# Optimization experiments

Measured on AMD Instinct MI355X. Metric: run time of the kernel, lower is better.

## Reference

```python
import jax, jax.numpy as jnp
import numpy as np

N, F, H, C = 8192, 512, 512, 64
SPARSITY = 0.5  # args.linear_sparsity


def _percentile(t, q):
    # torch kthvalue semantics: k = 1 + round(0.01*q*(n-1)), 1-indexed k-th smallest
    n = t.size
    k = int(1 + round(0.01 * q * (n - 1)))
    return jnp.sort(t.ravel())[k - 1]


def _pair_norm(x):
    x = x - x.mean(axis=0)
    rownorm_mean = jnp.sqrt(1e-6 + (x * x).sum(axis=1).mean())
    return x / rownorm_mean


def setup_inputs() -> dict:
    key = jax.random.key(0)
    ks = jax.random.split(key, 8)
    x = jax.random.normal(ks[0], (N, F), jnp.float32)
    adj = (jax.random.uniform(ks[1], (N, N)) < 0.002).astype(jnp.float32)
    W0 = jax.random.normal(ks[2], (H, F), jnp.float32) * (1.0 / np.sqrt(F))
    W1 = jax.random.normal(ks[3], (H, H), jnp.float32) * (1.0 / np.sqrt(H))
    W2 = jax.random.normal(ks[4], (C, H), jnp.float32) * (1.0 / np.sqrt(H))
    S0 = jax.random.normal(ks[5], (H, F), jnp.float32)
    S1 = jax.random.normal(ks[6], (H, H), jnp.float32)
    S2 = jax.random.normal(ks[7], (C, H), jnp.float32)
    return {"x": x, "adj": adj, "W0": W0, "W1": W1, "W2": W2,
            "S0": S0, "S1": S1, "S2": S2}


def reference(x, adj, W0, W1, W2, S0, S1, S2):
    # add self loops
    idx = jnp.arange(N)
    adj = adj.at[idx, idx].set(1.0)
    # global threshold over all |score| params (enable_abs_comp=True)
    all_scores = jnp.concatenate([jnp.abs(S0).ravel(), jnp.abs(S1).ravel(), jnp.abs(S2).ravel()])
    thr = _percentile(all_scores, SPARSITY * 100.0)
    # symmetric normalization D^-1/2 A D^-1/2
    deg_inv_sqrt = jnp.maximum(adj.sum(axis=-1), 1.0) ** -0.5
    adj_n = deg_inv_sqrt[:, None] * adj * deg_inv_sqrt[None, :]

    def masked_linear(h, W, S):
        Wm = W * (jnp.abs(S) > thr).astype(W.dtype)
        return h @ Wm.T

    # layers 0..num_layers-2 applied back-to-back (as in the source loop)
    h = masked_linear(x, W0, S0)
    h = masked_linear(h, W1, S1)
    h = adj_n @ h            # aggregation: [N,N] @ [N,H]
    h = _pair_norm(h)
    h = jax.nn.relu(h)
    h = masked_linear(h, W2, S2)
    return adj_n @ h          # [N, C]
```

## Files before the change

### kernel.cpp

```cpp
#include <hip/hip_runtime.h>
#include <hip/hip_bf16.h>

#define NN 8192
#define FF 512
#define HH 512
#define CC 64
#define NS_TOTAL 557056
#define KSEL 278529u
#define MAXNBR 96
#define MASKB 2176

typedef short short8 __attribute__((ext_vector_type(8)));
typedef __bf16 bf16x8 __attribute__((ext_vector_type(8)));
typedef float f32x4 __attribute__((ext_vector_type(4)));

__device__ inline unsigned short f2bf(float f) {
    unsigned u = __float_as_uint(f);
    u += 0x7fffu + ((u >> 16) & 1u);
    return (unsigned short)(u >> 16);
}
__device__ inline float bf2f(unsigned short h) {
    return __uint_as_float(((unsigned)h) << 16);
}

__device__ inline f32x4 mfma16x16x32(short8 a, short8 b, f32x4 c) {
    return __builtin_amdgcn_mfma_f32_16x16x32_bf16(
        __builtin_bit_cast(bf16x8, a), __builtin_bit_cast(bf16x8, b), c, 0, 0, 0);
}

__device__ inline void gload_lds16(const unsigned short* g, unsigned short* l) {
    __builtin_amdgcn_global_load_lds(
        (const __attribute__((address_space(1))) void*)g,
        (__attribute__((address_space(3))) void*)l,
        16, 0, 0);
}

__device__ void isel(const unsigned* __restrict__ hist, unsigned k,
                     unsigned& bin, unsigned& krem) {
    __shared__ unsigned sh[256];
    __shared__ unsigned res[2];
    const int t = threadIdx.x;
    __syncthreads();
    sh[t] = hist[t];
    __syncthreads();
    unsigned pre = 0;
    for (int i = 0; i < t; ++i) pre += sh[i];
    if (pre < k && k <= pre + sh[t]) { res[0] = (unsigned)t; res[1] = k - pre; }
    __syncthreads();
    bin = res[0]; krem = res[1];
}

__device__ void isel_chain(const unsigned* __restrict__ hists, int npass,
                           unsigned& prefix, unsigned& k) {
    prefix = 0; k = KSEL;
    for (int p = 0; p < npass; ++p) {
        unsigned bin, krem;
        isel(hists + p * 256, k, bin, krem);
        prefix |= bin << (24 - 8 * p);
        k = krem;
    }
}


__global__ __launch_bounds__(256) void hist8_kernel(const float* __restrict__ S0,
                                                    const float* __restrict__ S1,
                                                    const float* __restrict__ S2,
                                                    unsigned* __restrict__ hists, int pass) {
    unsigned prefix = 0, k;
    if (pass > 0) isel_chain(hists, pass, prefix, k);
    unsigned pmask = (pass > 0) ? (0xFFFFFFFFu << (32 - 8 * pass)) : 0u;
    int shift = 24 - 8 * pass;
    __shared__ unsigned lh[256];
    lh[threadIdx.x] = 0;
    __syncthreads();
    int stride = gridDim.x * blockDim.x;
    for (int idx = blockIdx.x * blockDim.x + threadIdx.x; idx < NS_TOTAL; idx += stride) {
        float v = (idx < 262144) ? S0[idx] : (idx < 524288) ? S1[idx - 262144] : S2[idx - 524288];
        unsigned key = __float_as_uint(fabsf(v));
        if ((key & pmask) == prefix)
            atomicAdd(&lh[(key >> shift) & 0xffu], 1u);
    }
    __syncthreads();
    unsigned c = lh[threadIdx.x];
    if (c) atomicAdd(&hists[pass * 256 + threadIdx.x], c);
}


__global__ __launch_bounds__(256) void mask_split_fused(
        const float* __restrict__ W0, const float* __restrict__ W1,
        const float* __restrict__ W2, const float* __restrict__ S0,
        const float* __restrict__ S1, const float* __restrict__ S2,
        const unsigned* __restrict__ hists,
        unsigned short* __restrict__ W0h, unsigned short* __restrict__ W0l,
        unsigned short* __restrict__ W1h, unsigned short* __restrict__ W1l,
        unsigned short* __restrict__ W2h, unsigned short* __restrict__ W2l,
        const float* __restrict__ X,
        unsigned short* __restrict__ Xh, unsigned short* __restrict__ Xl) {
    if (blockIdx.x >= MASKB) {
        int i = (blockIdx.x - MASKB) * 256 + threadIdx.x;
        float4 v = ((const float4*)X)[i];
        float vv[4] = {v.x, v.y, v.z, v.w};
        ushort4 hi, lo;
        unsigned short* hp = (unsigned short*)&hi;
        unsigned short* lp = (unsigned short*)&lo;
#pragma unroll
        for (int j = 0; j < 4; ++j) {
            hp[j] = f2bf(vv[j]);
            lp[j] = f2bf(vv[j] - bf2f(hp[j]));
        }
        *(ushort4*)&Xh[(size_t)i * 4] = hi;
        *(ushort4*)&Xl[(size_t)i * 4] = lo;
        return;
    }
    unsigned prefix, k;
    isel_chain(hists, 4, prefix, k);
    float thr = __uint_as_float(prefix);
    int idx = blockIdx.x * 256 + threadIdx.x;
    const float* W; const float* S; unsigned short* Yh; unsigned short* Yl; int i;
    if (idx < 262144)      { W = W0; S = S0; Yh = W0h; Yl = W0l; i = idx; }
    else if (idx < 524288) { W = W1; S = S1; Yh = W1h; Yl = W1l; i = idx - 262144; }
    else                   { W = W2; S = S2; Yh = W2h; Yl = W2l; i = idx - 524288; }
    float v = (fabsf(S[i]) > thr) ? W[i] : 0.f;
    unsigned short hi = f2bf(v);
    Yh[i] = hi;
    Yl[i] = f2bf(v - bf2f(hi));
}


template<int BMt, int BNt, int WRITE_SPLIT>
__global__ __launch_bounds__(256) void gemm_hl(
        const unsigned short* __restrict__ Ah, const unsigned short* __restrict__ Al,
        const unsigned short* __restrict__ Bh, const unsigned short* __restrict__ Bl,
        float* __restrict__ Cf, unsigned short* __restrict__ Ch,
        unsigned short* __restrict__ Cl, int Nn, int gridN, int gemmBlocks,
        const float* __restrict__ adj, int* __restrict__ nnz, int* __restrict__ colsI,
        float* __restrict__ dis, int degRow0) {
    constexpr int BK = 32;
    constexpr int MF = BMt / 32, NF = BNt / 32;
    __shared__ __align__(16) unsigned short AhS[BMt * BK], AlS[BMt * BK];
    __shared__ __align__(16) unsigned short BhS[BNt * BK], BlS[BNt * BK];
    __shared__ int dcnt;

    if ((int)blockIdx.x >= gemmBlocks) {
        int row = degRow0 + (int)blockIdx.x - gemmBlocks;
        if (threadIdx.x == 0) dcnt = 0;
        __syncthreads();
        const float4* arow = (const float4*)(adj + (size_t)row * NN);
        int* cp = colsI + (size_t)row * MAXNBR;
        for (int c4 = threadIdx.x; c4 < NN / 4; c4 += 256) {
            float4 v = arow[c4];
            int base = c4 * 4;
            float vv[4] = {v.x, v.y, v.z, v.w};
#pragma unroll
            for (int kq = 0; kq < 4; ++kq) {
                int col = base + kq;
                if (vv[kq] != 0.f || col == row) {
                    int s = atomicAdd(&dcnt, 1);
                    if (s < MAXNBR) cp[s] = col;
                }
            }
        }
        __syncthreads();
        if (threadIdx.x == 0) {
            int c = dcnt;
            nnz[row] = (c < MAXNBR) ? c : MAXNBR;
            dis[row] = rsqrtf((float)c);
        }
        return;
    }
    const int tid = threadIdx.x, lane = tid & 63, wid = tid >> 6;
    const int wr = wid >> 1, wc = wid & 1;
    const int bm = ((int)blockIdx.x / gridN) * BMt;
    const int bn = ((int)blockIdx.x % gridN) * BNt;
    const int r16 = lane & 15, kg = lane >> 4;
    const int srow = lane >> 2, scol = (lane & 3) * 8;
    constexpr int cA = BMt / 16, cB = BNt / 16, CPW = (2 * cA + 2 * cB) / 4;
    f32x4 acc[MF][NF] = {};

    for (int k0 = 0; k0 < 512; k0 += BK) {
        __syncthreads();
#pragma unroll
        for (int i = 0; i < CPW; ++i) {
            int c = wid * CPW + i;
            const unsigned short* src; unsigned short* dst; int cc, r0;
            if (c < cA)               { src = Ah; dst = AhS; cc = c;              r0 = bm + cc * 16; }
            else if (c < 2 * cA)      { src = Al; dst = AlS; cc = c - cA;         r0 = bm + cc * 16; }
            else if (c < 2 * cA + cB) { src = Bh; dst = BhS; cc = c - 2 * cA;     r0 = bn + cc * 16; }
            else                      { src = Bl; dst = BlS; cc = c - 2 * cA - cB; r0 = bn + cc * 16; }
            gload_lds16(src + (size_t)(r0 + srow) * 512 + k0 + scol, dst + cc * 512);
        }
        __syncthreads();
        const unsigned short* pAh = &AhS[(wr * (BMt / 2) + r16) * BK + kg * 8];
        const unsigned short* pAl = &AlS[(wr * (BMt / 2) + r16) * BK + kg * 8];
        const unsigned short* pBh = &BhS[(wc * (BNt / 2) + r16) * BK + kg * 8];
        const unsigned short* pBl = &BlS[(wc * (BNt / 2) + r16) * BK + kg * 8];
        short8 bh[NF], bl[NF];
#pragma unroll
        for (int n = 0; n < NF; ++n) {
            bh[n] = *(const short8*)(pBh + n * 16 * BK);
            bl[n] = *(const short8*)(pBl + n * 16 * BK);
        }
#pragma unroll
        for (int m = 0; m < MF; ++m) {
            short8 ah = *(const short8*)(pAh + m * 16 * BK);
            short8 al = *(const short8*)(pAl + m * 16 * BK);
#pragma unroll
            for (int n = 0; n < NF; ++n) {
                acc[m][n] = mfma16x16x32(ah, bh[n], acc[m][n]);
                acc[m][n] = mfma16x16x32(ah, bl[n], acc[m][n]);
                acc[m][n] = mfma16x16x32(al, bh[n], acc[m][n]);
            }
        }
    }
#pragma unroll
    for (int m = 0; m < MF; ++m) {
#pragma unroll
        for (int n = 0; n < NF; ++n) {
            int row0 = bm + wr * (BMt / 2) + m * 16 + kg * 4;
            int col  = bn + wc * (BNt / 2) + n * 16 + r16;
#pragma unroll
            for (int j = 0; j < 4; ++j) {
                float v = acc[m][n][j];
                if (WRITE_SPLIT) {
                    unsigned short hi = f2bf(v);
                    size_t base = (size_t)(row0 + j) * Nn + col;
                    Ch[base] = hi;
                    Cl[base] = f2bf(v - bf2f(hi));
                } else {
                    Cf[(size_t)(row0 + j) * Nn + col] = v;
                }
            }
        }
    }
}


__global__ void spmm512(const int* __restrict__ nnz, const int* __restrict__ colsI,
                        const float* __restrict__ dis, const float* __restrict__ Hin,
                        float* __restrict__ Hout) {
    int row = blockIdx.x;
    int t = threadIdx.x;
    int cnt = nnz[row];
    const int* cp = colsI + (size_t)row * MAXNBR;
    float4 acc = make_float4(0.f, 0.f, 0.f, 0.f);
    for (int j = 0; j < cnt; ++j) {
        int c = cp[j];
        float wgt = dis[c];
        float4 v = *(const float4*)(Hin + (size_t)c * HH + t * 4);
        acc.x += wgt * v.x; acc.y += wgt * v.y; acc.z += wgt * v.z; acc.w += wgt * v.w;
    }
    float di = dis[row];
    acc.x *= di; acc.y *= di; acc.z *= di; acc.w *= di;
    *(float4*)(Hout + (size_t)row * HH + t * 4) = acc;
}

__global__ void spmm64(const int* __restrict__ nnz, const int* __restrict__ colsI,
                       const float* __restrict__ dis, const float* __restrict__ Hin,
                       float* __restrict__ Hout) {
    int row = blockIdx.x;
    int t = threadIdx.x;
    int cnt = nnz[row];
    const int* cp = colsI + (size_t)row * MAXNBR;
    float acc = 0.f;
    for (int j = 0; j < cnt; ++j) {
        int c = cp[j];
        acc += dis[c] * Hin[(size_t)c * CC + t];
    }
    Hout[(size_t)row * CC + t] = dis[row] * acc;
}


__global__ void colstats_kernel(const float* __restrict__ X, float* __restrict__ colsum,
                                float* __restrict__ stats) {
    int t = threadIdx.x;
    float s0 = 0.f, s1 = 0.f, sq = 0.f;
    for (int r = blockIdx.x; r < NN; r += 256) {
        const float* row = X + (size_t)r * HH;
        float a = row[t], b = row[t + 256];
        s0 += a; s1 += b;
        sq += a * a + b * b;
    }
    atomicAdd(&colsum[t], s0);
    atomicAdd(&colsum[t + 256], s1);
#pragma unroll
    for (int o = 32; o > 0; o >>= 1) sq += __shfl_down(sq, o);
    __shared__ float red[4];
    int wv = t >> 6, lane = t & 63;
    if (lane == 0) red[wv] = sq;
    __syncthreads();
    if (t == 0) atomicAdd(stats, red[0] + red[1] + red[2] + red[3]);
}

__global__ __launch_bounds__(256) void pn_apply_split(const float* __restrict__ X,
                                                      const float* __restrict__ colsum,
                                                      const float* __restrict__ stats,
                                                      unsigned short* __restrict__ Yh,
                                                      unsigned short* __restrict__ Yl) {
    const float inv = 1.0f / (float)NN;
    int t = threadIdx.x;
    float c0 = colsum[t], c1 = colsum[t + 256];
    float sq = c0 * c0 + c1 * c1;
#pragma unroll
    for (int o = 32; o > 0; o >>= 1) sq += __shfl_down(sq, o);
    __shared__ float red[4];
    __shared__ float sbc;
    int wv = t >> 6, lane = t & 63;
    if (lane == 0) red[wv] = sq;
    __syncthreads();
    if (t == 0) {
        float msum = red[0] + red[1] + red[2] + red[3];
        sbc = 1.0f / sqrtf(1e-6f + (stats[0] - msum * inv) * inv);
    }
    __syncthreads();
    float s = sbc;

    int i = blockIdx.x * 256 + t;
    float4 v = ((const float4*)X)[i];
    float4 m = ((const float4*)colsum)[i & 127];
    float vv[4];
    vv[0] = fmaxf((v.x - m.x * inv) * s, 0.f);
    vv[1] = fmaxf((v.y - m.y * inv) * s, 0.f);
    vv[2] = fmaxf((v.z - m.z * inv) * s, 0.f);
    vv[3] = fmaxf((v.w - m.w * inv) * s, 0.f);
    ushort4 hi, lo;
    unsigned short* hp = (unsigned short*)&hi;
    unsigned short* lp = (unsigned short*)&lo;
#pragma unroll
    for (int j = 0; j < 4; ++j) {
        hp[j] = f2bf(vv[j]);
        lp[j] = f2bf(vv[j] - bf2f(hp[j]));
    }
    *(ushort4*)&Yh[(size_t)i * 4] = hi;
    *(ushort4*)&Yl[(size_t)i * 4] = lo;
}


extern "C" void kernel_launch(void* const* d_in, const int* in_sizes, int n_in,
                              void* d_out, int out_size, void* d_ws, size_t ws_size,
                              hipStream_t stream) {
    const float* x   = (const float*)d_in[0];
    const float* adj = (const float*)d_in[1];
    const float* W0  = (const float*)d_in[2];
    const float* W1  = (const float*)d_in[3];
    const float* W2  = (const float*)d_in[4];
    const float* S0  = (const float*)d_in[5];
    const float* S1  = (const float*)d_in[6];
    const float* S2  = (const float*)d_in[7];
    float* out = (float*)d_out;

    char* w = (char*)d_ws;
    size_t off = 0;
    auto alloc = [&](size_t b) { size_t r = off; off = (off + b + 255) & ~(size_t)255; return r; };
    unsigned* hists = (unsigned*)(w + alloc(4 * 256 * 4));
    float* colsum   = (float*)(w + alloc(HH * 4));
    float* stats    = (float*)(w + alloc(256));
    size_t zero_end = off;
    int* nnz   = (int*)(w + alloc(NN * 4));
    int* colsI = (int*)(w + alloc((size_t)NN * MAXNBR * 4));
    float* dis = (float*)(w + alloc(NN * 4));
    unsigned short* xh  = (unsigned short*)(w + alloc((size_t)NN * FF * 2));
    unsigned short* xl  = (unsigned short*)(w + alloc((size_t)NN * FF * 2));
    unsigned short* W0h = (unsigned short*)(w + alloc((size_t)HH * FF * 2));
    unsigned short* W0l = (unsigned short*)(w + alloc((size_t)HH * FF * 2));
    unsigned short* W1h = (unsigned short*)(w + alloc((size_t)HH * HH * 2));
    unsigned short* W1l = (unsigned short*)(w + alloc((size_t)HH * HH * 2));
    unsigned short* W2h = (unsigned short*)(w + alloc((size_t)CC * HH * 2));
    unsigned short* W2l = (unsigned short*)(w + alloc((size_t)CC * HH * 2));
    unsigned short* hAh = (unsigned short*)(w + alloc((size_t)NN * HH * 2));
    unsigned short* hAl = (unsigned short*)(w + alloc((size_t)NN * HH * 2));
    float* hB   = (float*)(w + alloc((size_t)NN * HH * 4));
    float* hAgg = (float*)(w + alloc((size_t)NN * HH * 4));
    unsigned short* hBh = (unsigned short*)(w + alloc((size_t)NN * HH * 2));
    unsigned short* hBl = (unsigned short*)(w + alloc((size_t)NN * HH * 2));
    float* h3   = (float*)(w + alloc((size_t)NN * CC * 4));
    (void)ws_size; (void)in_sizes; (void)n_in; (void)out_size;

    hipMemsetAsync(d_ws, 0, zero_end, stream);

    for (int p = 0; p < 4; ++p)
        hist8_kernel<<<256, 256, 0, stream>>>(S0, S1, S2, hists, p);

    mask_split_fused<<<MASKB + NN * FF / 4 / 256, 256, 0, stream>>>(
        W0, W1, W2, S0, S1, S2, hists, W0h, W0l, W1h, W1l, W2h, W2l, x, xh, xl);

    const int g12 = (NN / 64) * (HH / 128);
    gemm_hl<64, 128, 1><<<g12 + NN / 2, 256, 0, stream>>>(
        xh, xl, W0h, W0l, nullptr, hAh, hAl, HH, HH / 128, g12,
        adj, nnz, colsI, dis, 0);
    gemm_hl<64, 128, 0><<<g12 + NN / 2, 256, 0, stream>>>(
        hAh, hAl, W1h, W1l, hB, nullptr, nullptr, HH, HH / 128, g12,
        adj, nnz, colsI, dis, NN / 2);

    spmm512<<<NN, 128, 0, stream>>>(nnz, colsI, dis, hB, hAgg);

    colstats_kernel<<<256, 256, 0, stream>>>(hAgg, colsum, stats);
    pn_apply_split<<<(NN * HH / 4) / 256, 256, 0, stream>>>(hAgg, colsum, stats, hBh, hBl);

    const int g3 = (NN / 32) * (CC / 64);
    gemm_hl<32, 64, 0><<<g3, 256, 0, stream>>>(
        hBh, hBl, W2h, W2l, h3, nullptr, nullptr, CC, CC / 64, g3,
        nullptr, nullptr, nullptr, nullptr, 0);
    spmm64<<<NN, 64, 0, stream>>>(nnz, colsI, dis, h3, out);
}
```

Measured before the change: 246.0 us.

## Double-buffer LDS tiles in split-bf16 GEMM to overlap loads with MFMA

Gives the gemm_hl kernel two LDS buffers per operand tile, so the next K slice is staged into one buffer while MFMAs run on the other. This removes the barrier between each global-to-LDS load and its compute, hiding load latency. LDS use per block doubles, which may lower occupancy, and the loop is unrolled by two K steps.

```diff
diff --git a/kernel.cpp b/kernel.cpp
--- a/kernel.cpp
+++ b/kernel.cpp
@@ -137,8 +137,8 @@
         float* __restrict__ dis, int degRow0) {
     constexpr int BK = 32;
     constexpr int MF = BMt / 32, NF = BNt / 32;
-    __shared__ __align__(16) unsigned short AhS[BMt * BK], AlS[BMt * BK];
-    __shared__ __align__(16) unsigned short BhS[BNt * BK], BlS[BNt * BK];
+    __shared__ __align__(16) unsigned short AhS[2][BMt * BK], AlS[2][BMt * BK];
+    __shared__ __align__(16) unsigned short BhS[2][BNt * BK], BlS[2][BNt * BK];
     __shared__ int dcnt;
 
     if ((int)blockIdx.x >= gemmBlocks) {
@@ -177,40 +177,54 @@
     constexpr int cA = BMt / 16, cB = BNt / 16, CPW = (2 * cA + 2 * cB) / 4;
     f32x4 acc[MF][NF] = {};
 
-    for (int k0 = 0; k0 < 512; k0 += BK) {
-        __syncthreads();
+    auto STAGE = [&](unsigned short* ah, unsigned short* al,
+                     unsigned short* bh, unsigned short* bl, int k0) {
 #pragma unroll
         for (int i = 0; i < CPW; ++i) {
             int c = wid * CPW + i;
             const unsigned short* src; unsigned short* dst; int cc, r0;
-            if (c < cA)               { src = Ah; dst = AhS; cc = c;              r0 = bm + cc * 16; }
-            else if (c < 2 * cA)      { src = Al; dst = AlS; cc = c - cA;         r0 = bm + cc * 16; }
-            else if (c < 2 * cA + cB) { src = Bh; dst = BhS; cc = c - 2 * cA;     r0 = bn + cc * 16; }
-            else                      { src = Bl; dst = BlS; cc = c - 2 * cA - cB; r0 = bn + cc * 16; }
+            if (c < cA)               { src = Ah; dst = ah; cc = c;               r0 = bm + cc * 16; }
+            else if (c < 2 * cA)      { src = Al; dst = al; cc = c - cA;          r0 = bm + cc * 16; }
+            else if (c < 2 * cA + cB) { src = Bh; dst = bh; cc = c - 2 * cA;      r0 = bn + cc * 16; }
+            else                      { src = Bl; dst = bl; cc = c - 2 * cA - cB; r0 = bn + cc * 16; }
             gload_lds16(src + (size_t)(r0 + srow) * 512 + k0 + scol, dst + cc * 512);
         }
+    };
+    auto COMPUTE = [&](const unsigned short* ah, const unsigned short* al,
+                       const unsigned short* bh, const unsigned short* bl) {
+        const unsigned short* pAh = &ah[(wr * (BMt / 2) + r16) * BK + kg * 8];
+        const unsigned short* pAl = &al[(wr * (BMt / 2) + r16) * BK + kg * 8];
+        const unsigned short* pBh = &bh[(wc * (BNt / 2) + r16) * BK + kg * 8];
+        const unsigned short* pBl = &bl[(wc * (BNt / 2) + r16) * BK + kg * 8];
+        short8 bhf[NF], blf[NF];
+#pragma unroll
+        for (int n = 0; n < NF; ++n) {
+            bhf[n] = *(const short8*)(pBh + n * 16 * BK);
+            blf[n] = *(const short8*)(pBl + n * 16 * BK);
+        }
+#pragma unroll
+        for (int m = 0; m < MF; ++m) {
+            short8 ahf = *(const short8*)(pAh + m * 16 * BK);
+            short8 alf = *(const short8*)(pAl + m * 16 * BK);
+#pragma unroll
+            for (int n = 0; n < NF; ++n) {
+                acc[m][n] = mfma16x16x32(ahf, bhf[n], acc[m][n]);
+                acc[m][n] = mfma16x16x32(ahf, blf[n], acc[m][n]);
+                acc[m][n] = mfma16x16x32(alf, bhf[n], acc[m][n]);
+            }
+        }
+    };
+
+    STAGE(AhS[0], AlS[0], BhS[0], BlS[0], 0);
+    __syncthreads();
+    for (int k0 = 0; k0 < 512; k0 += 64) {
+        STAGE(AhS[1], AlS[1], BhS[1], BlS[1], k0 + 32);
+        COMPUTE(AhS[0], AlS[0], BhS[0], BlS[0]);
         __syncthreads();
-        const unsigned short* pAh = &AhS[(wr * (BMt / 2) + r16) * BK + kg * 8];
-        const unsigned short* pAl = &AlS[(wr * (BMt / 2) + r16) * BK + kg * 8];
-        const unsigned short* pBh = &BhS[(wc * (BNt / 2) + r16) * BK + kg * 8];
-        const unsigned short* pBl = &BlS[(wc * (BNt / 2) + r16) * BK + kg * 8];
-        short8 bh[NF], bl[NF];
-#pragma unroll
-        for (int n = 0; n < NF; ++n) {
-            bh[n] = *(const short8*)(pBh + n * 16 * BK);
-            bl[n] = *(const short8*)(pBl + n * 16 * BK);
-        }
-#pragma unroll
-        for (int m = 0; m < MF; ++m) {
-            short8 ah = *(const short8*)(pAh + m * 16 * BK);
-            short8 al = *(const short8*)(pAl + m * 16 * BK);
-#pragma unroll
-            for (int n = 0; n < NF; ++n) {
-                acc[m][n] = mfma16x16x32(ah, bh[n], acc[m][n]);
-                acc[m][n] = mfma16x16x32(ah, bl[n], acc[m][n]);
-                acc[m][n] = mfma16x16x32(al, bh[n], acc[m][n]);
-            }
-        }
+        if (k0 + 64 < 512)
+            STAGE(AhS[0], AlS[0], BhS[0], BlS[0], k0 + 64);
+        COMPUTE(AhS[1], AlS[1], BhS[1], BlS[1]);
+        __syncthreads();
     }
 #pragma unroll
     for (int m = 0; m < MF; ++m) {
```

Measured after the change: 257.0 us. +4.5%, slower.
